# Kernel tuning notes

Hardware: AMD Instinct MI355X
Metric: run time of the kernel (lower is better)

Reference implementation:

```python
import jax, jax.numpy as jnp
import numpy as np

HEAD_NUM = 8
EMB_SIZE = 768
B, N = 8, 1024


def setup_inputs() -> dict:
    key = jax.random.key(0)
    ks = jax.random.split(key, 9)
    s = 0.02
    return {
        "x": jax.random.normal(ks[0], (B, N, EMB_SIZE), dtype=jnp.float32),
        "Wq": jax.random.normal(ks[1], (EMB_SIZE, EMB_SIZE), dtype=jnp.float32) * s,
        "bq": jax.random.normal(ks[2], (EMB_SIZE,), dtype=jnp.float32) * s,
        "Wk": jax.random.normal(ks[3], (EMB_SIZE, EMB_SIZE), dtype=jnp.float32) * s,
        "bk": jax.random.normal(ks[4], (EMB_SIZE,), dtype=jnp.float32) * s,
        "Wv": jax.random.normal(ks[5], (EMB_SIZE, EMB_SIZE), dtype=jnp.float32) * s,
        "bv": jax.random.normal(ks[6], (EMB_SIZE,), dtype=jnp.float32) * s,
        "Wp": jax.random.normal(ks[7], (EMB_SIZE, EMB_SIZE), dtype=jnp.float32) * s,
        "bp": jax.random.normal(ks[8], (EMB_SIZE,), dtype=jnp.float32) * s,
    }


def reference(x, Wq, bq, Wk, bk, Wv, bv, Wp, bp):
    b, n, e = x.shape
    h = HEAD_NUM
    d = e // h
    # nn.Linear: y = x @ W^T + b
    q = (x @ Wq.T + bq).reshape(b, h, n, d)  # NOTE: raw reshape, as in source
    k = (x @ Wk.T + bk).reshape(b, h, n, d)
    v = (x @ Wv.T + bv).reshape(b, h, n, d)
    energy = jnp.einsum('bhqd,bhkd->bhqk', q, k)
    # source divides by sqrt(emb_size) AFTER softmax (faithful)
    attn = jax.nn.softmax(energy, axis=-1) / jnp.sqrt(jnp.float32(e))
    out = jnp.einsum('bhql,bhld->bhqd', attn, v).reshape(b, n, h * d)
    return out @ Wp.T + bp
```

## Files before the change

kernel.cpp:

```cpp
#include <hip/hip_runtime.h>
#include <hip/hip_bf16.h>


typedef __attribute__((ext_vector_type(8))) short short8;
typedef __attribute__((ext_vector_type(4))) float floatx4;
typedef __attribute__((ext_vector_type(16))) float floatx16;

static constexpr int EMB = 768;
static constexpr int SEQ = 1024;
static constexpr int DH = 96;
static constexpr int NBH = 64;
static constexpr int HEADBLK = SEQ * DH;
static constexpr int MROWS = 8192;
static constexpr int NW = EMB * EMB;
static constexpr int QKVN = 3 * EMB;

__device__ __forceinline__ unsigned bfround(float f) {
    unsigned u = __builtin_bit_cast(unsigned, f);
    return u + 0x7FFFu + ((u >> 16) & 1u);
}
__device__ __forceinline__ unsigned short f2bf(float f) {
    return (unsigned short)(bfround(f) >> 16);
}
__device__ __forceinline__ unsigned pk2(float lo, float hi) {
    return (bfround(lo) >> 16) | (bfround(hi) & 0xFFFF0000u);
}

__device__ __forceinline__ void gload16(const unsigned short* g, unsigned short* l) {
    __builtin_amdgcn_global_load_lds(
        (const __attribute__((address_space(1))) unsigned int*)g,
        (__attribute__((address_space(3))) unsigned int*)l, 16, 0, 0);
}

__global__ void cast_all(const float* __restrict__ x,
                         const float* __restrict__ Wq, const float* __restrict__ Wk,
                         const float* __restrict__ Wv, const float* __restrict__ Wp,
                         const float* __restrict__ bq, const float* __restrict__ bk,
                         const float* __restrict__ bv,
                         unsigned short* __restrict__ xb,
                         unsigned short* __restrict__ Wqkv, unsigned short* __restrict__ Wpb,
                         float* __restrict__ bias) {
    int bx = blockIdx.x;
    if (bx < 6144) {
        int i = bx * 1024 + threadIdx.x * 4;
        float4 v = *reinterpret_cast<const float4*>(x + i);
        ushort4 o;
        o.x = f2bf(v.x); o.y = f2bf(v.y); o.z = f2bf(v.z); o.w = f2bf(v.w);
        *reinterpret_cast<ushort4*>(xb + i) = o;
    } else if (bx < 8448) {
        int i4 = (bx - 6144) * 1024 + threadIdx.x * 4;
        const float* src;
        unsigned short* dst;
        if (i4 < 3 * NW) {
            int wi = i4 / NW;
            src = (wi == 0) ? Wq + i4 : (wi == 1) ? Wk + (i4 - NW) : Wv + (i4 - 2 * NW);
            dst = Wqkv + i4;
        } else {
            src = Wp + (i4 - 3 * NW);
            dst = Wpb + (i4 - 3 * NW);
        }
        float4 v = *reinterpret_cast<const float4*>(src);
        ushort4 o;
        o.x = f2bf(v.x); o.y = f2bf(v.y); o.z = f2bf(v.z); o.w = f2bf(v.w);
        *reinterpret_cast<ushort4*>(dst) = o;
    } else {
        int j = (bx - 8448) * 256 + threadIdx.x;
        if (j < QKVN)
            bias[j] = (j < 768) ? bq[j] : (j < 1536) ? bk[j - 768] : bv[j - 1536];
    }
}

__global__ __launch_bounds__(256) void gemm_qkv(
    const unsigned short* __restrict__ A,
    const unsigned short* __restrict__ Bm,
    const float* __restrict__ bias,
    unsigned short* __restrict__ Qo,
    unsigned short* __restrict__ Ko,
    unsigned short* __restrict__ Vo) {
    __shared__ unsigned short As[128 * 64];
    __shared__ unsigned short Bs[128 * 64];
    const int K = EMB;

    const int t = threadIdx.x;
    const int lane = t & 63;
    const int w = t >> 6;
    const int wm = (w >> 1) * 64;
    const int wn = (w & 1) * 64;
    const int l32 = lane & 31;
    const int lh = lane >> 5;
    const int bm = blockIdx.x * 128;
    const int by = blockIdx.y;
    const int bn = by * 128;

    const unsigned short* Agp[4];
    const unsigned short* Bgp[4];
#pragma unroll
    for (int i = 0; i < 4; i++) {
        int f = i * 2048 + w * 512 + lane * 8;
        int row = f >> 6;
        int cc = (f >> 3) & 7;
        int gk = (cc ^ (row & 7)) * 8;
        Agp[i] = A + (size_t)(bm + row) * K + gk;
        Bgp[i] = Bm + (size_t)(bn + row) * K + gk;
    }

    floatx16 acc[2][2];
#pragma unroll
    for (int i = 0; i < 2; i++)
#pragma unroll
        for (int j = 0; j < 2; j++)
#pragma unroll
            for (int r = 0; r < 16; r++) acc[i][j][r] = 0.0f;

    const int sx = lane & 7;
    for (int k0 = 0; k0 < K; k0 += 64) {
        __syncthreads();
#pragma unroll
        for (int i = 0; i < 4; i++) {
            gload16(Agp[i] + k0, As + i * 2048 + w * 512);
            gload16(Bgp[i] + k0, Bs + i * 2048 + w * 512);
        }
        __syncthreads();

#pragma unroll
        for (int ks = 0; ks < 4; ks++) {
            const int co = ((ks * 2 + lh) ^ sx) * 8;
            short8 af[2], bfr[2];
#pragma unroll
            for (int mt = 0; mt < 2; mt++)
                af[mt] = *reinterpret_cast<const short8*>(As + (wm + mt * 32 + l32) * 64 + co);
#pragma unroll
            for (int nt = 0; nt < 2; nt++)
                bfr[nt] = *reinterpret_cast<const short8*>(Bs + (wn + nt * 32 + l32) * 64 + co);
#pragma unroll
            for (int mt = 0; mt < 2; mt++)
#pragma unroll
                for (int nt = 0; nt < 2; nt++)
                    acc[mt][nt] = __builtin_amdgcn_mfma_f32_32x32x16_bf16(af[mt], bfr[nt], acc[mt][nt], 0, 0, 0);
        }
    }

    unsigned short* dst = (by < 6) ? Qo : (by < 12) ? Ko : Vo;
    const int bnl = (by % 6) * 128;
#pragma unroll
    for (int mt = 0; mt < 2; mt++) {
#pragma unroll
        for (int nt = 0; nt < 2; nt++) {
            int colg = bn + wn + nt * 32 + l32;
            int coll = bnl + wn + nt * 32 + l32;
            float bb = bias[colg];
#pragma unroll
            for (int rg = 0; rg < 4; rg++) {
                int rowb = bm + wm + mt * 32 + rg * 8 + lh * 4;
#pragma unroll
                for (int rr = 0; rr < 4; rr++)
                    dst[(size_t)(rowb + rr) * EMB + coll] = f2bf(acc[mt][nt][rg * 4 + rr] + bb);
            }
        }
    }
}

__global__ __launch_bounds__(256) void gemm_proj(
    const unsigned short* __restrict__ A,
    const unsigned short* __restrict__ Bm,
    const float* __restrict__ bias,
    float* __restrict__ C) {
    __shared__ unsigned short As[64 * 64];
    __shared__ unsigned short Bs[128 * 64];
    const int K = EMB, N = EMB;

    const int t = threadIdx.x;
    const int lane = t & 63;
    const int w = t >> 6;
    const int wm = (w >> 1) * 32;
    const int wn = (w & 1) * 64;
    const int l32 = lane & 31;
    const int lh = lane >> 5;
    const int bm = blockIdx.x * 64;
    const int bn = blockIdx.y * 128;

    const unsigned short* Agp[2];
    const unsigned short* Bgp[4];
#pragma unroll
    for (int i = 0; i < 2; i++) {
        int f = i * 2048 + w * 512 + lane * 8;
        int row = f >> 6;
        int cc = (f >> 3) & 7;
        Agp[i] = A + (size_t)(bm + row) * K + ((cc ^ (row & 7)) * 8);
    }
#pragma unroll
    for (int i = 0; i < 4; i++) {
        int f = i * 2048 + w * 512 + lane * 8;
        int row = f >> 6;
        int cc = (f >> 3) & 7;
        Bgp[i] = Bm + (size_t)(bn + row) * K + ((cc ^ (row & 7)) * 8);
    }

    floatx16 acc[2];
#pragma unroll
    for (int j = 0; j < 2; j++)
#pragma unroll
        for (int r = 0; r < 16; r++) acc[j][r] = 0.0f;

    const int sx = lane & 7;
    for (int k0 = 0; k0 < K; k0 += 64) {
        __syncthreads();
#pragma unroll
        for (int i = 0; i < 2; i++) gload16(Agp[i] + k0, As + i * 2048 + w * 512);
#pragma unroll
        for (int i = 0; i < 4; i++) gload16(Bgp[i] + k0, Bs + i * 2048 + w * 512);
        __syncthreads();

#pragma unroll
        for (int ks = 0; ks < 4; ks++) {
            const int co = ((ks * 2 + lh) ^ sx) * 8;
            short8 af = *reinterpret_cast<const short8*>(As + (wm + l32) * 64 + co);
            short8 bfr[2];
#pragma unroll
            for (int nt = 0; nt < 2; nt++)
                bfr[nt] = *reinterpret_cast<const short8*>(Bs + (wn + nt * 32 + l32) * 64 + co);
#pragma unroll
            for (int nt = 0; nt < 2; nt++)
                acc[nt] = __builtin_amdgcn_mfma_f32_32x32x16_bf16(af, bfr[nt], acc[nt], 0, 0, 0);
        }
    }

#pragma unroll
    for (int nt = 0; nt < 2; nt++) {
        int col = bn + wn + nt * 32 + l32;
        float bb = bias[col];
#pragma unroll
        for (int rg = 0; rg < 4; rg++) {
            int rowb = bm + wm + rg * 8 + lh * 4;
#pragma unroll
            for (int rr = 0; rr < 4; rr++)
                C[(size_t)(rowb + rr) * N + col] = acc[nt][rg * 4 + rr] + bb;
        }
    }
}

__global__ __launch_bounds__(256) void transpose_v(const unsigned short* __restrict__ V,
                                                   unsigned short* __restrict__ Vt) {
    __shared__ unsigned short L[64 * 104];
    const int t = threadIdx.x;
    const int bh = blockIdx.x, nb = blockIdx.y;
    const unsigned short* Vg = V + (size_t)bh * HEADBLK + (size_t)nb * 64 * DH;
#pragma unroll
    for (int i = 0; i < 3; i++) {
        int f = i * 2048 + t * 8;
        int r = f / 96, c = f - r * 96;
        *reinterpret_cast<short8*>(L + r * 104 + c) = *reinterpret_cast<const short8*>(Vg + f);
    }
    __syncthreads();
    unsigned short* dst = Vt + (size_t)bh * HEADBLK;
#pragma unroll
    for (int i = 0; i < 3; i++) {
        int f = i * 2048 + t * 8;
        int d = f >> 6, c = f & 63;
        int base = (c & 32) + ((c >> 3) & 3) * 4;
        union { short8 s; unsigned short u[8]; } o;
#pragma unroll
        for (int j = 0; j < 8; j++) {
            int key = base + ((j & 4) << 2) + (j & 3);
            o.u[j] = L[key * 104 + d];
        }
        *reinterpret_cast<short8*>(dst + d * SEQ + nb * 64 + c) = o.s;
    }
}

__global__ __launch_bounds__(256, 4) void attn_kernel(
    const unsigned short* __restrict__ Q,
    const unsigned short* __restrict__ K,
    const unsigned short* __restrict__ Vt,
    unsigned short* __restrict__ O) {
    __shared__ unsigned short Ks[64 * 104];
    __shared__ unsigned short Vs[96 * 72];

    const int t = threadIdx.x;
    const int lane = t & 63;
    const int w = t >> 6;
    const int lrow = lane & 15;
    const int quad = lane >> 4;
    const int bh = blockIdx.x, qb = blockIdx.y;

    const unsigned short* Qh = Q + (size_t)bh * HEADBLK;
    const unsigned short* Kh = K + (size_t)bh * HEADBLK;
    const unsigned short* Vth = Vt + (size_t)bh * HEADBLK;

    short8 qf[3];
    {
        const unsigned short* qsrc = Qh + (size_t)(qb * 64 + w * 16 + lrow) * DH + quad * 8;
#pragma unroll
        for (int ks = 0; ks < 3; ks++)
            qf[ks] = *reinterpret_cast<const short8*>(qsrc + ks * 32);
    }

    const unsigned short* Kp[3];
    const unsigned short* Vp[3];
    unsigned short* KsW[3];
    unsigned short* VsW[3];
#pragma unroll
    for (int i = 0; i < 3; i++) {
        int f = i * 2048 + t * 8;
        int r = f / 96, c = f - r * 96;
        Kp[i] = Kh + f;
        KsW[i] = Ks + r * 104 + c;
        int d = f >> 6, cv = f & 63;
        Vp[i] = Vth + d * SEQ + cv;
        VsW[i] = Vs + d * 72 + cv;
    }

    short8 kreg[3], vreg[3];
#pragma unroll
    for (int i = 0; i < 3; i++) {
        kreg[i] = *reinterpret_cast<const short8*>(Kp[i]);
        vreg[i] = *reinterpret_cast<const short8*>(Vp[i]);
    }

    float l_ = 0.0f;
    floatx4 acco[6];
#pragma unroll
    for (int n = 0; n < 6; n++)
#pragma unroll
        for (int r = 0; r < 4; r++) acco[n][r] = 0.0f;

    for (int kb = 0; kb < 16; kb++) {
        __syncthreads();
#pragma unroll
        for (int i = 0; i < 3; i++) {
            *reinterpret_cast<short8*>(KsW[i]) = kreg[i];
            *reinterpret_cast<short8*>(VsW[i]) = vreg[i];
        }
        __syncthreads();
        if (kb < 15) {
#pragma unroll
            for (int i = 0; i < 3; i++) {
                kreg[i] = *reinterpret_cast<const short8*>(Kp[i] + (kb + 1) * 6144);
                vreg[i] = *reinterpret_cast<const short8*>(Vp[i] + (kb + 1) * 64);
            }
        }

        floatx4 sacc[4];
#pragma unroll
        for (int kt = 0; kt < 4; kt++)
#pragma unroll
            for (int r = 0; r < 4; r++) sacc[kt][r] = 0.0f;
#pragma unroll
        for (int ks = 0; ks < 3; ks++) {
#pragma unroll
            for (int kt = 0; kt < 4; kt++) {
                short8 ak = *reinterpret_cast<const short8*>(
                    Ks + (kt * 16 + lrow) * 104 + ks * 32 + quad * 8);
                sacc[kt] = __builtin_amdgcn_mfma_f32_16x16x32_bf16(ak, qf[ks], sacc[kt], 0, 0, 0);
            }
        }

        float rs = 0.0f;
        unsigned pk01[4], pk23[4];
#pragma unroll
        for (int kt = 0; kt < 4; kt++) {
            float p0 = __expf(sacc[kt][0]);
            float p1 = __expf(sacc[kt][1]);
            float p2 = __expf(sacc[kt][2]);
            float p3 = __expf(sacc[kt][3]);
            rs += (p0 + p1) + (p2 + p3);
            pk01[kt] = pk2(p0, p1);
            pk23[kt] = pk2(p2, p3);
        }
        rs += __shfl_xor(rs, 16);
        rs += __shfl_xor(rs, 32);
        l_ += rs;

#pragma unroll
        for (int s = 0; s < 2; s++) {
            union { short8 s8; unsigned u[4]; } bp;
            bp.u[0] = pk01[2 * s];
            bp.u[1] = pk23[2 * s];
            bp.u[2] = pk01[2 * s + 1];
            bp.u[3] = pk23[2 * s + 1];
#pragma unroll
            for (int n = 0; n < 6; n++) {
                short8 av = *reinterpret_cast<const short8*>(
                    Vs + (n * 16 + lrow) * 72 + s * 32 + quad * 8);
                acco[n] = __builtin_amdgcn_mfma_f32_16x16x32_bf16(av, bp.s8, acco[n], 0, 0, 0);
            }
        }
    }

    const float inv_sqrt_e = 0.036084391824351615f;
    float invl = inv_sqrt_e / l_;
    unsigned short* dst = O + (size_t)bh * HEADBLK +
                          (size_t)(qb * 64 + w * 16 + lrow) * DH;
#pragma unroll
    for (int n = 0; n < 6; n++) {
        uint2 o2;
        o2.x = pk2(acco[n][0] * invl, acco[n][1] * invl);
        o2.y = pk2(acco[n][2] * invl, acco[n][3] * invl);
        *reinterpret_cast<uint2*>(dst + n * 16 + quad * 4) = o2;
    }
}

extern "C" void kernel_launch(void* const* d_in, const int* in_sizes, int n_in,
                              void* d_out, int out_size, void* d_ws, size_t ws_size,
                              hipStream_t stream) {
    const float* x = (const float*)d_in[0];
    const float* Wq = (const float*)d_in[1];
    const float* bq = (const float*)d_in[2];
    const float* Wk = (const float*)d_in[3];
    const float* bk = (const float*)d_in[4];
    const float* Wv = (const float*)d_in[5];
    const float* bv = (const float*)d_in[6];
    const float* Wp = (const float*)d_in[7];
    const float* bp = (const float*)d_in[8];
    float* out = (float*)d_out;

    char* ws = (char*)d_ws;
    size_t off = 0;
    auto alloc = [&](size_t bytes) {
        char* p = ws + off;
        off += (bytes + 255) & ~(size_t)255;
        return p;
    };
    const int nx = MROWS * EMB;
    unsigned short* xb    = (unsigned short*)alloc((size_t)nx * 2);
    unsigned short* Wqkvb = (unsigned short*)alloc((size_t)3 * NW * 2);
    unsigned short* Wpb   = (unsigned short*)alloc((size_t)NW * 2);
    float*          biasq = (float*)alloc((size_t)QKVN * 4);
    unsigned short* Qb    = (unsigned short*)alloc((size_t)nx * 2);
    unsigned short* Kb    = (unsigned short*)alloc((size_t)nx * 2);
    unsigned short* Vb    = (unsigned short*)alloc((size_t)nx * 2);
    unsigned short* Vtb   = (unsigned short*)alloc((size_t)nx * 2);
    unsigned short* Ob    = (unsigned short*)alloc((size_t)nx * 2);

    cast_all<<<8457, 256, 0, stream>>>(x, Wq, Wk, Wv, Wp, bq, bk, bv,
                                       xb, Wqkvb, Wpb, biasq);

    gemm_qkv<<<dim3(MROWS / 128, QKVN / 128), 256, 0, stream>>>(
        xb, Wqkvb, biasq, Qb, Kb, Vb);

    transpose_v<<<dim3(NBH, SEQ / 64), 256, 0, stream>>>(Vb, Vtb);

    attn_kernel<<<dim3(NBH, SEQ / 64), 256, 0, stream>>>(Qb, Kb, Vtb, Ob);

    gemm_proj<<<dim3(MROWS / 64, EMB / 128), 256, 0, stream>>>(Ob, Wpb, bp, out);
}
```

Before: 194.3 us.

## Switch attention to 32x32x16 MFMA with 128-query blocks

Reworks the attention kernel to use 32x32x16 bf16 MFMA tiles, so each wave handles 32 query rows and a block covers 128 queries instead of 64. The V transpose permutation is changed to match the new P-operand layout. This halves the number of blocks and doubles the query rows per K/V tile load, reducing LDS and global traffic per query and the MFMA instruction count. In exchange, the larger accumulators raise register pressure (launch bounds relaxed to 2 blocks per SM) and the grid shrinks to 512 blocks.

```diff
diff --git a/kernel.cpp b/kernel.cpp
--- a/kernel.cpp
+++ b/kernel.cpp
@@ -256,19 +256,19 @@
 #pragma unroll
     for (int i = 0; i < 3; i++) {
         int f = i * 2048 + t * 8;
-        int d = f >> 6, c = f & 63;
-        int base = (c & 32) + ((c >> 3) & 3) * 4;
+        int d = f >> 6, c0 = f & 63;
         union { short8 s; unsigned short u[8]; } o;
 #pragma unroll
         for (int j = 0; j < 8; j++) {
-            int key = base + ((j & 4) << 2) + (j & 3);
+            int c = c0 + j;
+            int key = (c & ~12) | ((c & 4) << 1) | ((c & 8) >> 1);
             o.u[j] = L[key * 104 + d];
         }
-        *reinterpret_cast<short8*>(dst + d * SEQ + nb * 64 + c) = o.s;
-    }
-}
-
-__global__ __launch_bounds__(256, 4) void attn_kernel(
+        *reinterpret_cast<short8*>(dst + d * SEQ + nb * 64 + c0) = o.s;
+    }
+}
+
+__global__ __launch_bounds__(256, 2) void attn_kernel(
     const unsigned short* __restrict__ Q,
     const unsigned short* __restrict__ K,
     const unsigned short* __restrict__ Vt,
@@ -279,20 +279,20 @@
     const int t = threadIdx.x;
     const int lane = t & 63;
     const int w = t >> 6;
-    const int lrow = lane & 15;
-    const int quad = lane >> 4;
+    const int l32 = lane & 31;
+    const int lh = lane >> 5;
     const int bh = blockIdx.x, qb = blockIdx.y;
 
     const unsigned short* Qh = Q + (size_t)bh * HEADBLK;
     const unsigned short* Kh = K + (size_t)bh * HEADBLK;
     const unsigned short* Vth = Vt + (size_t)bh * HEADBLK;
 
-    short8 qf[3];
+    short8 qf[6];
     {
-        const unsigned short* qsrc = Qh + (size_t)(qb * 64 + w * 16 + lrow) * DH + quad * 8;
-#pragma unroll
-        for (int ks = 0; ks < 3; ks++)
-            qf[ks] = *reinterpret_cast<const short8*>(qsrc + ks * 32);
+        const unsigned short* qsrc = Qh + (size_t)(qb * 128 + w * 32 + l32) * DH + lh * 8;
+#pragma unroll
+        for (int ks = 0; ks < 6; ks++)
+            qf[ks] = *reinterpret_cast<const short8*>(qsrc + ks * 16);
     }
 
     const unsigned short* Kp[3];
@@ -318,11 +318,11 @@
     }
 
     float l_ = 0.0f;
-    floatx4 acco[6];
-#pragma unroll
-    for (int n = 0; n < 6; n++)
-#pragma unroll
-        for (int r = 0; r < 4; r++) acco[n][r] = 0.0f;
+    floatx16 acco[3];
+#pragma unroll
+    for (int n = 0; n < 3; n++)
+#pragma unroll
+        for (int r = 0; r < 16; r++) acco[n][r] = 0.0f;
 
     for (int kb = 0; kb < 16; kb++) {
         __syncthreads();
@@ -340,49 +340,46 @@
             }
         }
 
-        floatx4 sacc[4];
-#pragma unroll
-        for (int kt = 0; kt < 4; kt++)
-#pragma unroll
-            for (int r = 0; r < 4; r++) sacc[kt][r] = 0.0f;
-#pragma unroll
-        for (int ks = 0; ks < 3; ks++) {
-#pragma unroll
-            for (int kt = 0; kt < 4; kt++) {
+        floatx16 sacc[2];
+#pragma unroll
+        for (int kt = 0; kt < 2; kt++)
+#pragma unroll
+            for (int r = 0; r < 16; r++) sacc[kt][r] = 0.0f;
+
+#pragma unroll
+        for (int ks = 0; ks < 6; ks++) {
+#pragma unroll
+            for (int kt = 0; kt < 2; kt++) {
                 short8 ak = *reinterpret_cast<const short8*>(
-                    Ks + (kt * 16 + lrow) * 104 + ks * 32 + quad * 8);
-                sacc[kt] = __builtin_amdgcn_mfma_f32_16x16x32_bf16(ak, qf[ks], sacc[kt], 0, 0, 0);
+                    Ks + (kt * 32 + l32) * 104 + ks * 16 + lh * 8);
+                sacc[kt] = __builtin_amdgcn_mfma_f32_32x32x16_bf16(ak, qf[ks], sacc[kt], 0, 0, 0);
             }
         }
 
         float rs = 0.0f;
-        unsigned pk01[4], pk23[4];
-#pragma unroll
-        for (int kt = 0; kt < 4; kt++) {
-            float p0 = __expf(sacc[kt][0]);
-            float p1 = __expf(sacc[kt][1]);
-            float p2 = __expf(sacc[kt][2]);
-            float p3 = __expf(sacc[kt][3]);
-            rs += (p0 + p1) + (p2 + p3);
-            pk01[kt] = pk2(p0, p1);
-            pk23[kt] = pk2(p2, p3);
-        }
-        rs += __shfl_xor(rs, 16);
+#pragma unroll
+        for (int kt = 0; kt < 2; kt++)
+#pragma unroll
+            for (int r = 0; r < 16; r++) {
+                float v = __expf(sacc[kt][r]);
+                sacc[kt][r] = v;
+                rs += v;
+            }
         rs += __shfl_xor(rs, 32);
         l_ += rs;
 
 #pragma unroll
-        for (int s = 0; s < 2; s++) {
+        for (int kt2 = 0; kt2 < 4; kt2++) {
+            const int kt = kt2 >> 1, ro = (kt2 & 1) * 8;
             union { short8 s8; unsigned u[4]; } bp;
-            bp.u[0] = pk01[2 * s];
-            bp.u[1] = pk23[2 * s];
-            bp.u[2] = pk01[2 * s + 1];
-            bp.u[3] = pk23[2 * s + 1];
-#pragma unroll
-            for (int n = 0; n < 6; n++) {
+#pragma unroll
+            for (int p = 0; p < 4; p++)
+                bp.u[p] = pk2(sacc[kt][ro + 2 * p], sacc[kt][ro + 2 * p + 1]);
+#pragma unroll
+            for (int n = 0; n < 3; n++) {
                 short8 av = *reinterpret_cast<const short8*>(
-                    Vs + (n * 16 + lrow) * 72 + s * 32 + quad * 8);
-                acco[n] = __builtin_amdgcn_mfma_f32_16x16x32_bf16(av, bp.s8, acco[n], 0, 0, 0);
+                    Vs + (n * 32 + l32) * 72 + kt2 * 16 + lh * 8);
+                acco[n] = __builtin_amdgcn_mfma_f32_32x32x16_bf16(av, bp.s8, acco[n], 0, 0, 0);
             }
         }
     }
@@ -390,13 +387,16 @@
     const float inv_sqrt_e = 0.036084391824351615f;
     float invl = inv_sqrt_e / l_;
     unsigned short* dst = O + (size_t)bh * HEADBLK +
-                          (size_t)(qb * 64 + w * 16 + lrow) * DH;
-#pragma unroll
-    for (int n = 0; n < 6; n++) {
-        uint2 o2;
-        o2.x = pk2(acco[n][0] * invl, acco[n][1] * invl);
-        o2.y = pk2(acco[n][2] * invl, acco[n][3] * invl);
-        *reinterpret_cast<uint2*>(dst + n * 16 + quad * 4) = o2;
+                          (size_t)(qb * 128 + w * 32 + l32) * DH + lh * 4;
+#pragma unroll
+    for (int n = 0; n < 3; n++) {
+#pragma unroll
+        for (int rg = 0; rg < 4; rg++) {
+            uint2 o2;
+            o2.x = pk2(acco[n][rg * 4 + 0] * invl, acco[n][rg * 4 + 1] * invl);
+            o2.y = pk2(acco[n][rg * 4 + 2] * invl, acco[n][rg * 4 + 3] * invl);
+            *reinterpret_cast<uint2*>(dst + n * 32 + rg * 8) = o2;
+        }
     }
 }
 
@@ -440,7 +440,7 @@
 
     transpose_v<<<dim3(NBH, SEQ / 64), 256, 0, stream>>>(Vb, Vtb);
 
-    attn_kernel<<<dim3(NBH, SEQ / 64), 256, 0, stream>>>(Qb, Kb, Vtb, Ob);
+    attn_kernel<<<dim3(NBH, SEQ / 128), 256, 0, stream>>>(Qb, Kb, Vtb, Ob);
 
     gemm_proj<<<dim3(MROWS / 64, EMB / 128), 256, 0, stream>>>(Ob, Wpb, bp, out);
 }
```

Measured after the change: 188.7 us. 2.9% less time.
